# Kernel optimization log

Hardware: AMD Instinct MI355X
Metric: run time of the kernel (lower is better)

The kernel has to match this reference:

```python
import jax, jax.numpy as jnp
import numpy as np

# Hard-coded constants from the original module
GAMMA = 0.1      # self.gamma default
N_STEPS = 10     # self.n_steps default
RHO = 0.9        # RMSProp decay
LR = 0.009       # RMSProp learning rate
MOM = 0.9        # momentum
EPS = 1e-8       # RMSProp epsilon
ABS_EPS = 1e-6   # diff_abs smoothing: diff_abs(x) = sqrt(x^2 + 1e-6)

B, IN_DIM, OUT_DIM = 4096, 2048, 4096


def setup_inputs() -> dict:
    key = jax.random.key(0)
    k1, k2 = jax.random.split(key)
    inputs = jax.random.normal(k1, (B, IN_DIM), dtype=jnp.float32)
    # keras 'uniform' init: U(-0.05, 0.05), shape (output_dim, input_dim)
    W = jax.random.uniform(k2, (OUT_DIM, IN_DIM), minval=-0.05, maxval=0.05, dtype=jnp.float32)
    return {"inputs": inputs, "W": W}


def reference(inputs, W):
    batch = inputs.shape[0]
    out_dim = W.shape[0]
    a = jnp.sqrt(inputs * inputs + ABS_EPS)          # diff_abs(inputs), [B, in_dim]
    act = lambda u: 0.5 * (1.0 + jnp.exp(-u))        # self.activation

    def cost(x):
        # l1_norm.sum() + l1_inov + own_norm  (prior = 0)
        l1 = (GAMMA * act(x @ W) * a).sum()
        l1_inov = (GAMMA / 10.0) * jnp.sum(x * x)
        own = GAMMA * jnp.sum(jnp.sqrt(x * x + ABS_EPS))
        return l1 + l1_inov + own

    grad_cost = jax.grad(cost)

    def step(carry, _):
        x, acc1, acc2 = carry
        g = grad_cost(x)                              # [B, out_dim]
        new_acc1 = RHO * acc1 + (1.0 - RHO) * g * g
        denom = jnp.sqrt(new_acc1 + EPS)
        new_acc2 = MOM * acc2 - LR * g / denom
        cand = x - LR * g / denom
        t = 0.1 * LR / denom                          # elementwise prox threshold
        new_x = jnp.maximum(cand - t, 0.0) + jnp.minimum(cand + t, 0.0) + MOM * new_acc2
        new_x = jax.lax.stop_gradient(new_x)          # theano disconnected_grad
        return (new_x, new_acc1, new_acc2), None

    z = jnp.zeros((batch, out_dim), dtype=inputs.dtype)
    # scan runs n_steps; last step's l1_norm uses the state after n_steps-1 updates,
    # so run n_steps-1 updates then compute the final l1_norm directly.
    (x, _, _), _ = jax.lax.scan(step, (z, z, z), None, length=N_STEPS - 1)
    return GAMMA * act(x @ W) * a                     # outputs[-1][-1]: last l1_norm, [B, in_dim]
```

## Files before the change

kernel.cpp:

```cpp
#include <hip/hip_runtime.h>
#include <cstdint>
#include <cstddef>

#define B_DIM   4096
#define IN_DIM  2048
#define OUT_DIM 4096

typedef __attribute__((ext_vector_type(8))) __bf16 bf16x8;
typedef __attribute__((ext_vector_type(4))) float  f32x4;
typedef unsigned short ushortT;

__device__ __forceinline__ ushortT f2bf(float f) {
    unsigned int u = __float_as_uint(f);
    u += 0x7FFFu + ((u >> 16) & 1u);
    return (ushortT)(u >> 16);
}
__device__ __forceinline__ float bf2f(ushortT b) {
    return __uint_as_float(((unsigned int)b) << 16);
}

__device__ __forceinline__ void gload16(const void* g, void* l) {
    __builtin_amdgcn_global_load_lds(
        (const __attribute__((address_space(1))) void*)g,
        (__attribute__((address_space(3))) void*)l, 16, 0, 0);
}

__global__ void prep_g0_kernel(const float* __restrict__ in, ushortT* __restrict__ Gb,
                               ushortT* __restrict__ negA) {
    int i = blockIdx.x * 256 + threadIdx.x;
    float4 v = reinterpret_cast<const float4*>(in)[i];
    ushort4 g;
    g.x = f2bf(-0.05f * sqrtf(v.x * v.x + 1e-6f));
    g.y = f2bf(-0.05f * sqrtf(v.y * v.y + 1e-6f));
    g.z = f2bf(-0.05f * sqrtf(v.z * v.z + 1e-6f));
    g.w = f2bf(-0.05f * sqrtf(v.w * v.w + 1e-6f));
    reinterpret_cast<ushort4*>(Gb)[i]   = g;
    reinterpret_cast<ushort4*>(negA)[i] = g;
}

__global__ void conv_w_kernel(const float* __restrict__ W, ushortT* __restrict__ Wb,
                              ushortT* __restrict__ WTb) {
    __shared__ float tile[64][65];
    const int i0 = blockIdx.x * 64;
    const int j0 = blockIdx.y * 64;
    const int c  = threadIdx.x & 63;
    const int rq = threadIdx.x >> 6;
#pragma unroll
    for (int rp = 0; rp < 16; ++rp) {
        int row = rp * 4 + rq;
        float w = W[(size_t)(j0 + row) * IN_DIM + i0 + c];
        tile[row][c] = w;
        Wb[(size_t)(j0 + row) * IN_DIM + i0 + c] = f2bf(w);
    }
    __syncthreads();
#pragma unroll
    for (int rp = 0; rp < 16; ++rp) {
        int row = rp * 4 + rq;
        WTb[(size_t)(i0 + row) * OUT_DIM + j0 + c] = f2bf(tile[c][row]);
    }
}

#define EPILOGUE(MR_)                                                          \
    float* lep = (float*)(smem + w * 4352);                                    \
    const int li = lane >> 4;                                                  \
    const int lc = lane & 15;                                                  \
    _Pragma("unroll")                                                          \
    for (int m = 0; m < (MR_); ++m) {                                          \
        _Pragma("unroll")                                                      \
        for (int n = 0; n < 4; ++n)                                            \
            _Pragma("unroll")                                                  \
            for (int i = 0; i < 4; ++i)                                        \
                lep[(li * 4 + i) * 68 + n * 16 + lc] = acc[m][n][i];           \
        asm volatile("s_waitcnt lgkmcnt(0)" ::: "memory");                     \
        __builtin_amdgcn_sched_barrier(0);                                     \
        _Pragma("unroll")                                                      \
        for (int rr = 0; rr < 4; ++rr) {                                       \
            const int row = rr + li * 4;                                       \
            float4 v = *reinterpret_cast<const float4*>(&lep[row * 68 + lc * 4]); \
            const size_t idx  = (size_t)(row0w + m * 16 + row) * N + col0w + lc * 4; \
            const size_t idx4 = idx >> 2;                                      \
            if constexpr (EPI == 0) {                                          \
                ushort4 au = *reinterpret_cast<const ushort4*>(&nega[idx]);    \
                ushort4 g;                                                     \
                g.x = f2bf(bf2f(au.x) * __expf(-v.x));                         \
                g.y = f2bf(bf2f(au.y) * __expf(-v.y));                         \
                g.z = f2bf(bf2f(au.z) * __expf(-v.z));                         \
                g.w = f2bf(bf2f(au.w) * __expf(-v.w));                         \
                *reinterpret_cast<ushort4*>(&Gb[idx]) = g;                     \
            } else if constexpr (EPI == 1) {                                   \
                float4 iv = reinterpret_cast<const float4*>(inb)[idx4];        \
                float4 o;                                                      \
                o.x = 0.05f * (1.0f + expf(-v.x)) * sqrtf(iv.x * iv.x + 1e-6f); \
                o.y = 0.05f * (1.0f + expf(-v.y)) * sqrtf(iv.y * iv.y + 1e-6f); \
                o.z = 0.05f * (1.0f + expf(-v.z)) * sqrtf(iv.z * iv.z + 1e-6f); \
                o.w = 0.05f * (1.0f + expf(-v.w)) * sqrtf(iv.w * iv.w + 1e-6f); \
                reinterpret_cast<float4*>(out)[idx4] = o;                      \
            } else if constexpr (EPI == 3) {                                   \
                float vs[4] = {v.x, v.y, v.z, v.w};                            \
                ushortT a1n[4], a2n[4], xbn[4];                                \
                _Pragma("unroll")                                              \
                for (int j = 0; j < 4; ++j) {                                  \
                    float g    = vs[j];                                        \
                    float a1   = 0.1f * g * g;                                 \
                    float inv  = rsqrtf(a1 + 1e-8f);                           \
                    float r_   = 0.009f * g * inv;                             \
                    float a2   = -r_;                                          \
                    float cand = -r_;                                          \
                    float t_   = 0.0009f * inv;                                \
                    float xn   = fmaxf(cand - t_, 0.0f) + fminf(cand + t_, 0.0f) + 0.9f * a2; \
                    a1n[j] = f2bf(a1); a2n[j] = f2bf(a2); xbn[j] = f2bf(xn);   \
                }                                                              \
                *reinterpret_cast<ushort4*>(&acc1[idx]) = make_ushort4(a1n[0], a1n[1], a1n[2], a1n[3]); \
                *reinterpret_cast<ushort4*>(&acc2[idx]) = make_ushort4(a2n[0], a2n[1], a2n[2], a2n[3]); \
                *reinterpret_cast<ushort4*>(&xb[idx])   = make_ushort4(xbn[0], xbn[1], xbn[2], xbn[3]); \
            } else {                                                           \
                ushort4 xu  = *reinterpret_cast<const ushort4*>(&xb[idx]);     \
                ushort4 a1u = *reinterpret_cast<const ushort4*>(&acc1[idx]);   \
                ushort4 a2u = *reinterpret_cast<const ushort4*>(&acc2[idx]);   \
                float xs[4] = {bf2f(xu.x), bf2f(xu.y), bf2f(xu.z), bf2f(xu.w)}; \
                float vs[4] = {v.x, v.y, v.z, v.w};                            \
                ushortT a1s[4] = {a1u.x, a1u.y, a1u.z, a1u.w};                 \
                ushortT a2s[4] = {a2u.x, a2u.y, a2u.z, a2u.w};                 \
                ushortT a1n[4], a2n[4], xbn[4];                                \
                _Pragma("unroll")                                              \
                for (int j = 0; j < 4; ++j) {                                  \
                    float g    = vs[j] + 0.02f * xs[j] + 0.1f * xs[j] * rsqrtf(xs[j] * xs[j] + 1e-6f); \
                    float a1   = 0.9f * bf2f(a1s[j]) + 0.1f * g * g;           \
                    float inv  = rsqrtf(a1 + 1e-8f);                           \
                    float r_   = 0.009f * g * inv;                             \
                    float a2   = 0.9f * bf2f(a2s[j]) - r_;                     \
                    float cand = xs[j] - r_;                                   \
                    float t_   = 0.0009f * inv;                                \
                    float xn   = fmaxf(cand - t_, 0.0f) + fminf(cand + t_, 0.0f) + 0.9f * a2; \
                    a1n[j] = f2bf(a1); a2n[j] = f2bf(a2); xbn[j] = f2bf(xn);   \
                }                                                              \
                *reinterpret_cast<ushort4*>(&acc1[idx]) = make_ushort4(a1n[0], a1n[1], a1n[2], a1n[3]); \
                *reinterpret_cast<ushort4*>(&acc2[idx]) = make_ushort4(a2n[0], a2n[1], a2n[2], a2n[3]); \
                *reinterpret_cast<ushort4*>(&xb[idx])   = make_ushort4(xbn[0], xbn[1], xbn[2], xbn[3]); \
            }                                                                  \
        }                                                                      \
        asm volatile("s_waitcnt lgkmcnt(0)" ::: "memory");                     \
    }

#define PHASE(MB, RB, SLOTP, STTILE, C0, NC)                                   \
    {                                                                          \
        const char* sb_ = (SLOTP);                                             \
        if (RB) {                                                              \
            _Pragma("unroll")                                                  \
            for (int n = 0; n < 4; ++n)                                        \
                bF[n] = *reinterpret_cast<const bf16x8*>(sb_ + bRd[n]);        \
        }                                                                      \
        bf16x8 aF[4];                                                          \
        _Pragma("unroll")                                                      \
        for (int m = 0; m < 4; ++m)                                            \
            aF[m] = *reinterpret_cast<const bf16x8*>(sb_ + aRd[m]);            \
        if ((STTILE) < nt) {                                                   \
            _Pragma("unroll")                                                  \
            for (int c = 0; c < (NC); ++c) stage_chunk((STTILE), (C0) + c);    \
        }                                                                      \
        __builtin_amdgcn_sched_barrier(0);                                     \
        __builtin_amdgcn_s_barrier();                                          \
        asm volatile("s_waitcnt lgkmcnt(0)" ::: "memory");                     \
        __builtin_amdgcn_sched_barrier(0);                                     \
        __builtin_amdgcn_s_setprio(1);                                         \
        _Pragma("unroll")                                                      \
        for (int m = 0; m < 4; ++m) {                                          \
            _Pragma("unroll")                                                  \
            for (int n = 0; n < 4; ++n)                                        \
                acc[m][n] = __builtin_amdgcn_mfma_f32_16x16x32_bf16(           \
                    aF[m], bF[n], acc[m][n], 0, 0, 0);                         \
        }                                                                      \
        __builtin_amdgcn_s_setprio(0);                                         \
        __builtin_amdgcn_s_barrier();                                          \
        __builtin_amdgcn_sched_barrier(0);                                     \
    }

template <int EPI>
__global__ __launch_bounds__(512, 1)
void gemm_phase(const ushortT* __restrict__ A, const ushortT* __restrict__ Bm,
                int N, int K,
                const float* __restrict__ inb, const ushortT* __restrict__ nega,
                ushortT* __restrict__ Gb, float* __restrict__ out,
                ushortT* __restrict__ acc1, ushortT* __restrict__ acc2,
                ushortT* __restrict__ xb) {
    constexpr int BM = 128, BN = 256;
    constexpr int ASZ  = BM * 64;
    constexpr int SLOT = ASZ + BN * 64;
    constexpr int LA   = 1, LB = 2, L = 3;
    __shared__ alignas(16) char smem[4 * SLOT];

    const int tid  = threadIdx.x;
    const int lane = tid & 63;
    const int w    = tid >> 6;
    const int wm   = w >> 2;
    const int wn   = w & 3;
    const int nbx  = N / BN;
    const int nwg  = gridDim.x;
    const int cpx  = nwg >> 3;
    const int bid  = (int)blockIdx.x;
    const int swz  = (bid & 7) * cpx + (bid >> 3);
    const int bx   = swz % nbx;
    const int by   = swz / nbx;
    const int row0 = by * BM;
    const int col0 = bx * BN;
    const size_t strideK2 = (size_t)K * 2;

    const char* gp[L]; int lo[L];
#pragma unroll
    for (int i = 0; i < LA; ++i) {
        int Lp  = i * 512 + tid;
        int row = Lp >> 2, sl = Lp & 3;
        int src = sl ^ ((row >> 1) & 3);
        gp[i] = (const char*)A + (size_t)(row0 + row) * strideK2 + src * 16;
        lo[i] = i * 8192 + w * 1024;
    }
#pragma unroll
    for (int i = 0; i < LB; ++i) {
        int Lp  = i * 512 + tid;
        int row = Lp >> 2, sl = Lp & 3;
        int src = sl ^ ((row >> 1) & 3);
        gp[LA + i] = (const char*)Bm + (size_t)(col0 + row) * strideK2 + src * 16;
        lo[LA + i] = ASZ + i * 8192 + w * 1024;
    }
    auto stage_all = [&](int tt) {
        char* sb = smem + (tt & 3) * SLOT;
        const size_t kb = (size_t)tt * 64;
#pragma unroll
        for (int c = 0; c < L; ++c) gload16(gp[c] + kb, sb + lo[c]);
    };
    auto stage_chunk = [&](int tt, int c) {
        gload16(gp[c] + (size_t)tt * 64, smem + (tt & 3) * SLOT + lo[c]);
    };

    int aRd[4], bRd[4];
#pragma unroll
    for (int m = 0; m < 4; ++m) {
        int row = wm * 64 + m * 16 + (lane & 15);
        aRd[m] = row * 64 + (((lane >> 4) ^ ((row >> 1) & 3)) * 16);
    }
#pragma unroll
    for (int n = 0; n < 4; ++n) {
        int row = wn * 64 + n * 16 + (lane & 15);
        bRd[n] = ASZ + row * 64 + (((lane >> 4) ^ ((row >> 1) & 3)) * 16);
    }

    f32x4 acc[4][4] = {};
    const int nt = K >> 5;

    stage_all(0); stage_all(1); stage_all(2);

    for (int tt = 0; tt < nt; tt += 2) {
        if (tt + 2 < nt) asm volatile("s_waitcnt vmcnt(%0)" :: "n"(L) : "memory");
        else             asm volatile("s_waitcnt vmcnt(0)"  ::: "memory");
        __builtin_amdgcn_s_barrier();
        __builtin_amdgcn_sched_barrier(0);

        const char* sb0 = smem + (tt & 3) * SLOT;
        const char* sb1 = smem + ((tt + 1) & 3) * SLOT;
        bf16x8 bF[4];
        PHASE(0, true, sb0, tt + 3, 0, 3)
        PHASE(0, true, sb1, tt + 4, 0, 3)
    }

    __builtin_amdgcn_s_barrier();
    const int row0w = row0 + wm * 64;
    const int col0w = col0 + wn * 64;
    EPILOGUE(4)
}

template <int EPI>
__global__ __launch_bounds__(512, 4)
void gemm_mb(const ushortT* __restrict__ A, const ushortT* __restrict__ Bm,
             int N, int K,
             const float* __restrict__ inb, const ushortT* __restrict__ nega,
             ushortT* __restrict__ Gb, float* __restrict__ out,
             ushortT* __restrict__ acc1, ushortT* __restrict__ acc2,
             ushortT* __restrict__ xb) {
    constexpr int BM = 256, BN = 128;
    constexpr int ASZ  = BM * 64;
    constexpr int SLOT = ASZ + BN * 64;
    constexpr int CA   = 2, CB = 1, L = 3;
    __shared__ alignas(16) char smem[3 * SLOT];

    const int tid  = threadIdx.x;
    const int lane = tid & 63;
    const int w    = tid >> 6;
    const int wm   = w >> 1;
    const int wn   = w & 1;
    const int nbx  = N / BN;
    const int nwg  = gridDim.x;
    const int cpx  = nwg >> 3;
    const int bid  = (int)blockIdx.x;
    const int swz  = (bid & 7) * cpx + (bid >> 3);
    const int bx   = swz % nbx;
    const int by   = swz / nbx;
    const int row0 = by * BM;
    const int col0 = bx * BN;
    const size_t strideK2 = (size_t)K * 2;

    const char* gp[L]; int lo[L];
#pragma unroll
    for (int c = 0; c < CA; ++c) {
        int Lp  = c * 512 + tid;
        int row = Lp >> 2, sl = Lp & 3;
        int src = sl ^ ((row >> 1) & 3);
        gp[c] = (const char*)A + (size_t)(row0 + row) * strideK2 + src * 16;
        lo[c] = c * 8192 + w * 1024;
    }
#pragma unroll
    for (int c = 0; c < CB; ++c) {
        int Lp  = c * 512 + tid;
        int row = Lp >> 2, sl = Lp & 3;
        int src = sl ^ ((row >> 1) & 3);
        gp[CA + c] = (const char*)Bm + (size_t)(col0 + row) * strideK2 + src * 16;
        lo[CA + c] = ASZ + c * 8192 + w * 1024;
    }
    auto stage = [&](int tt) {
        char* sb = smem + (tt % 3) * SLOT;
        const size_t kb = (size_t)tt * 64;
#pragma unroll
        for (int c = 0; c < L; ++c) gload16(gp[c] + kb, sb + lo[c]);
    };

    int aRd[4], bRd[4];
#pragma unroll
    for (int m = 0; m < 4; ++m) {
        int row = wm * 64 + m * 16 + (lane & 15);
        aRd[m] = row * 64 + (((lane >> 4) ^ ((row >> 1) & 3)) * 16);
    }
#pragma unroll
    for (int n = 0; n < 4; ++n) {
        int row = wn * 64 + n * 16 + (lane & 15);
        bRd[n] = ASZ + row * 64 + (((lane >> 4) ^ ((row >> 1) & 3)) * 16);
    }

    f32x4 acc[4][4] = {};
    const int nt = K >> 5;

    stage(0); stage(1);

    for (int tt = 0; tt < nt; ++tt) {
        if (tt < nt - 1) asm volatile("s_waitcnt vmcnt(%0)" :: "n"(L) : "memory");
        else             asm volatile("s_waitcnt vmcnt(0)"  ::: "memory");
        __builtin_amdgcn_s_barrier();
        __builtin_amdgcn_sched_barrier(0);

        const char* sb = smem + (tt % 3) * SLOT;
        bf16x8 aF[4], bF[4];
#pragma unroll
        for (int n = 0; n < 4; ++n) bF[n] = *reinterpret_cast<const bf16x8*>(sb + bRd[n]);
#pragma unroll
        for (int m = 0; m < 4; ++m) aF[m] = *reinterpret_cast<const bf16x8*>(sb + aRd[m]);
        if (tt + 2 < nt) stage(tt + 2);
        __builtin_amdgcn_s_setprio(1);
#pragma unroll
        for (int m = 0; m < 4; ++m)
#pragma unroll
            for (int n = 0; n < 4; ++n)
                acc[m][n] = __builtin_amdgcn_mfma_f32_16x16x32_bf16(aF[m], bF[n], acc[m][n], 0, 0, 0);
        __builtin_amdgcn_s_setprio(0);
    }

    __builtin_amdgcn_s_barrier();
    const int row0w = row0 + wm * 64;
    const int col0w = col0 + wn * 64;
    EPILOGUE(4)
}

extern "C" void kernel_launch(void* const* d_in, const int* in_sizes, int n_in,
                              void* d_out, int out_size, void* d_ws, size_t ws_size,
                              hipStream_t stream) {
    const float* in = (const float*)d_in[0];
    const float* W  = (const float*)d_in[1];
    float* out = (float*)d_out;
    char* ws = (char*)d_ws;

    ushortT* acc1 = (ushortT*)(ws);
    ushortT* acc2 = (ushortT*)(ws + ((size_t)32  << 20));
    ushortT* xb   = (ushortT*)(ws + ((size_t)64  << 20));
    ushortT* Wb   = (ushortT*)(ws + ((size_t)96  << 20));
    ushortT* WTb  = (ushortT*)(ws + ((size_t)112 << 20));
    ushortT* Gb   = (ushortT*)(ws + ((size_t)128 << 20));
    ushortT* negA = (ushortT*)(ws + ((size_t)144 << 20));


    prep_g0_kernel<<<dim3(B_DIM * IN_DIM / 4 / 256), dim3(256), 0, stream>>>(in, Gb, negA);
    conv_w_kernel<<<dim3(IN_DIM / 64, OUT_DIM / 64), dim3(256), 0, stream>>>(W, Wb, WTb);

    gemm_mb<3><<<dim3(512), dim3(512), 0, stream>>>(
        Gb, Wb, OUT_DIM, IN_DIM, nullptr, nullptr, nullptr, nullptr, acc1, acc2, xb);
    for (int step = 1; step < 9; ++step) {
        gemm_phase<0><<<dim3(256), dim3(512), 0, stream>>>(
            xb, WTb, IN_DIM, OUT_DIM, nullptr, negA, Gb, nullptr, nullptr, nullptr, nullptr);
        gemm_mb<2><<<dim3(512), dim3(512), 0, stream>>>(
            Gb, Wb, OUT_DIM, IN_DIM, nullptr, nullptr, nullptr, nullptr, acc1, acc2, xb);
    }
    gemm_phase<1><<<dim3(256), dim3(512), 0, stream>>>(
        xb, WTb, IN_DIM, OUT_DIM, in, nullptr, nullptr, out, nullptr, nullptr, nullptr);
}
```

Measured before the change: 1.533 ms.

## Load A operand fragments directly from global memory, staging only B in LDS

Both GEMM kernels now read the A-operand MFMA fragments straight from global memory into registers each k-tile, and use LDS only for the B operand. This shrinks LDS footprint and shared-memory traffic and removes the A staging loads. The cost is that A loads become uncoalesced per-lane 16-byte global reads that sit on the critical path before the MFMAs with no prefetch depth. gemm_da also adds a barrier at the end of every iteration.

```diff
diff --git a/kernel.cpp b/kernel.cpp
--- a/kernel.cpp
+++ b/kernel.cpp
@@ -142,21 +142,19 @@
         asm volatile("s_waitcnt lgkmcnt(0)" ::: "memory");                     \
     }
 
-#define PHASE(MB, RB, SLOTP, STTILE, C0, NC)                                   \
+#define PHASE_DA(TK, SLOTP, STTILE)                                            \
     {                                                                          \
         const char* sb_ = (SLOTP);                                             \
-        if (RB) {                                                              \
-            _Pragma("unroll")                                                  \
-            for (int n = 0; n < 4; ++n)                                        \
-                bF[n] = *reinterpret_cast<const bf16x8*>(sb_ + bRd[n]);        \
-        }                                                                      \
-        bf16x8 aF[4];                                                          \
+        bf16x8 aF[4], bF[4];                                                   \
         _Pragma("unroll")                                                      \
         for (int m = 0; m < 4; ++m)                                            \
-            aF[m] = *reinterpret_cast<const bf16x8*>(sb_ + aRd[m]);            \
+            aF[m] = *reinterpret_cast<const bf16x8*>(gAf[m] + (size_t)(TK) * 64); \
+        _Pragma("unroll")                                                      \
+        for (int n = 0; n < 4; ++n)                                            \
+            bF[n] = *reinterpret_cast<const bf16x8*>(sb_ + bRd[n]);            \
         if ((STTILE) < nt) {                                                   \
-            _Pragma("unroll")                                                  \
-            for (int c = 0; c < (NC); ++c) stage_chunk((STTILE), (C0) + c);    \
+            gload16(gp[0] + (size_t)(STTILE) * 64, smem + ((STTILE) & 3) * SLOT + lo[0]); \
+            gload16(gp[1] + (size_t)(STTILE) * 64, smem + ((STTILE) & 3) * SLOT + lo[1]); \
         }                                                                      \
         __builtin_amdgcn_sched_barrier(0);                                     \
         __builtin_amdgcn_s_barrier();                                          \
@@ -184,9 +182,7 @@
                 ushortT* __restrict__ acc1, ushortT* __restrict__ acc2,
                 ushortT* __restrict__ xb) {
     constexpr int BM = 128, BN = 256;
-    constexpr int ASZ  = BM * 64;
-    constexpr int SLOT = ASZ + BN * 64;
-    constexpr int LA   = 1, LB = 2, L = 3;
+    constexpr int SLOT = BN * 64;
     __shared__ alignas(16) char smem[4 * SLOT];
 
     const int tid  = threadIdx.x;
@@ -205,43 +201,33 @@
     const int col0 = bx * BN;
     const size_t strideK2 = (size_t)K * 2;
 
-    const char* gp[L]; int lo[L];
-#pragma unroll
-    for (int i = 0; i < LA; ++i) {
+    const char* gp[2]; int lo[2];
+#pragma unroll
+    for (int i = 0; i < 2; ++i) {
         int Lp  = i * 512 + tid;
         int row = Lp >> 2, sl = Lp & 3;
         int src = sl ^ ((row >> 1) & 3);
-        gp[i] = (const char*)A + (size_t)(row0 + row) * strideK2 + src * 16;
+        gp[i] = (const char*)Bm + (size_t)(col0 + row) * strideK2 + src * 16;
         lo[i] = i * 8192 + w * 1024;
-    }
-#pragma unroll
-    for (int i = 0; i < LB; ++i) {
-        int Lp  = i * 512 + tid;
-        int row = Lp >> 2, sl = Lp & 3;
-        int src = sl ^ ((row >> 1) & 3);
-        gp[LA + i] = (const char*)Bm + (size_t)(col0 + row) * strideK2 + src * 16;
-        lo[LA + i] = ASZ + i * 8192 + w * 1024;
     }
     auto stage_all = [&](int tt) {
         char* sb = smem + (tt & 3) * SLOT;
         const size_t kb = (size_t)tt * 64;
-#pragma unroll
-        for (int c = 0; c < L; ++c) gload16(gp[c] + kb, sb + lo[c]);
+        gload16(gp[0] + kb, sb + lo[0]);
+        gload16(gp[1] + kb, sb + lo[1]);
     };
-    auto stage_chunk = [&](int tt, int c) {
-        gload16(gp[c] + (size_t)tt * 64, smem + (tt & 3) * SLOT + lo[c]);
-    };
-
-    int aRd[4], bRd[4];
-#pragma unroll
-    for (int m = 0; m < 4; ++m) {
-        int row = wm * 64 + m * 16 + (lane & 15);
-        aRd[m] = row * 64 + (((lane >> 4) ^ ((row >> 1) & 3)) * 16);
-    }
+
+    int bRd[4];
 #pragma unroll
     for (int n = 0; n < 4; ++n) {
         int row = wn * 64 + n * 16 + (lane & 15);
-        bRd[n] = ASZ + row * 64 + (((lane >> 4) ^ ((row >> 1) & 3)) * 16);
+        bRd[n] = row * 64 + (((lane >> 4) ^ ((row >> 1) & 3)) * 16);
+    }
+    const char* gAf[4];
+#pragma unroll
+    for (int m = 0; m < 4; ++m) {
+        int rowA = row0 + wm * 64 + m * 16 + (lane & 15);
+        gAf[m] = (const char*)A + (size_t)rowA * strideK2 + (lane >> 4) * 16;
     }
 
     f32x4 acc[4][4] = {};
@@ -250,16 +236,15 @@
     stage_all(0); stage_all(1); stage_all(2);
 
     for (int tt = 0; tt < nt; tt += 2) {
-        if (tt + 2 < nt) asm volatile("s_waitcnt vmcnt(%0)" :: "n"(L) : "memory");
-        else             asm volatile("s_waitcnt vmcnt(0)"  ::: "memory");
+        if (tt + 2 < nt) asm volatile("s_waitcnt vmcnt(2)" ::: "memory");
+        else             asm volatile("s_waitcnt vmcnt(0)" ::: "memory");
         __builtin_amdgcn_s_barrier();
         __builtin_amdgcn_sched_barrier(0);
 
         const char* sb0 = smem + (tt & 3) * SLOT;
         const char* sb1 = smem + ((tt + 1) & 3) * SLOT;
-        bf16x8 bF[4];
-        PHASE(0, true, sb0, tt + 3, 0, 3)
-        PHASE(0, true, sb1, tt + 4, 0, 3)
+        PHASE_DA(tt,     sb0, tt + 3)
+        PHASE_DA(tt + 1, sb1, tt + 4)
     }
 
     __builtin_amdgcn_s_barrier();
@@ -270,17 +255,15 @@
 
 template <int EPI>
 __global__ __launch_bounds__(512, 4)
-void gemm_mb(const ushortT* __restrict__ A, const ushortT* __restrict__ Bm,
+void gemm_da(const ushortT* __restrict__ A, const ushortT* __restrict__ Bm,
              int N, int K,
              const float* __restrict__ inb, const ushortT* __restrict__ nega,
              ushortT* __restrict__ Gb, float* __restrict__ out,
              ushortT* __restrict__ acc1, ushortT* __restrict__ acc2,
              ushortT* __restrict__ xb) {
     constexpr int BM = 256, BN = 128;
-    constexpr int ASZ  = BM * 64;
-    constexpr int SLOT = ASZ + BN * 64;
-    constexpr int CA   = 2, CB = 1, L = 3;
-    __shared__ alignas(16) char smem[3 * SLOT];
+    constexpr int BSZ = BN * 64;
+    __shared__ alignas(16) char smem[34816];
 
     const int tid  = threadIdx.x;
     const int lane = tid & 63;
@@ -298,60 +281,49 @@
     const int col0 = bx * BN;
     const size_t strideK2 = (size_t)K * 2;
 
-    const char* gp[L]; int lo[L];
-#pragma unroll
-    for (int c = 0; c < CA; ++c) {
-        int Lp  = c * 512 + tid;
-        int row = Lp >> 2, sl = Lp & 3;
-        int src = sl ^ ((row >> 1) & 3);
-        gp[c] = (const char*)A + (size_t)(row0 + row) * strideK2 + src * 16;
-        lo[c] = c * 8192 + w * 1024;
-    }
-#pragma unroll
-    for (int c = 0; c < CB; ++c) {
-        int Lp  = c * 512 + tid;
-        int row = Lp >> 2, sl = Lp & 3;
-        int src = sl ^ ((row >> 1) & 3);
-        gp[CA + c] = (const char*)Bm + (size_t)(col0 + row) * strideK2 + src * 16;
-        lo[CA + c] = ASZ + c * 8192 + w * 1024;
-    }
-    auto stage = [&](int tt) {
-        char* sb = smem + (tt % 3) * SLOT;
-        const size_t kb = (size_t)tt * 64;
-#pragma unroll
-        for (int c = 0; c < L; ++c) gload16(gp[c] + kb, sb + lo[c]);
+    {
+    }
+    const int rowS = tid >> 2;
+    const int srcS = (tid & 3) ^ ((rowS >> 1) & 3);
+    const char* gB = (const char*)Bm + (size_t)(col0 + rowS) * strideK2 + srcS * 16;
+    const int loB = w * 1024;
+    auto stageB = [&](int tt) {
+        gload16(gB + (size_t)tt * 64, smem + (tt % 3) * BSZ + loB);
     };
 
-    int aRd[4], bRd[4];
-#pragma unroll
-    for (int m = 0; m < 4; ++m) {
-        int row = wm * 64 + m * 16 + (lane & 15);
-        aRd[m] = row * 64 + (((lane >> 4) ^ ((row >> 1) & 3)) * 16);
-    }
+    int bRd[4];
 #pragma unroll
     for (int n = 0; n < 4; ++n) {
         int row = wn * 64 + n * 16 + (lane & 15);
-        bRd[n] = ASZ + row * 64 + (((lane >> 4) ^ ((row >> 1) & 3)) * 16);
+        bRd[n] = row * 64 + (((lane >> 4) ^ ((row >> 1) & 3)) * 16);
+    }
+    const char* gAf[4];
+#pragma unroll
+    for (int m = 0; m < 4; ++m) {
+        int rowA = row0 + wm * 64 + m * 16 + (lane & 15);
+        gAf[m] = (const char*)A + (size_t)rowA * strideK2 + (lane >> 4) * 16;
     }
 
     f32x4 acc[4][4] = {};
     const int nt = K >> 5;
 
-    stage(0); stage(1);
+    stageB(0); stageB(1);
 
     for (int tt = 0; tt < nt; ++tt) {
-        if (tt < nt - 1) asm volatile("s_waitcnt vmcnt(%0)" :: "n"(L) : "memory");
-        else             asm volatile("s_waitcnt vmcnt(0)"  ::: "memory");
+        if (tt < nt - 1) asm volatile("s_waitcnt vmcnt(1)" ::: "memory");
+        else             asm volatile("s_waitcnt vmcnt(0)" ::: "memory");
         __builtin_amdgcn_s_barrier();
         __builtin_amdgcn_sched_barrier(0);
 
-        const char* sb = smem + (tt % 3) * SLOT;
+        const char* sb = smem + (tt % 3) * BSZ;
         bf16x8 aF[4], bF[4];
 #pragma unroll
-        for (int n = 0; n < 4; ++n) bF[n] = *reinterpret_cast<const bf16x8*>(sb + bRd[n]);
-#pragma unroll
-        for (int m = 0; m < 4; ++m) aF[m] = *reinterpret_cast<const bf16x8*>(sb + aRd[m]);
-        if (tt + 2 < nt) stage(tt + 2);
+        for (int m = 0; m < 4; ++m)
+            aF[m] = *reinterpret_cast<const bf16x8*>(gAf[m] + (size_t)tt * 64);
+#pragma unroll
+        for (int n = 0; n < 4; ++n)
+            bF[n] = *reinterpret_cast<const bf16x8*>(sb + bRd[n]);
+        if (tt + 2 < nt) stageB(tt + 2);
         __builtin_amdgcn_s_setprio(1);
 #pragma unroll
         for (int m = 0; m < 4; ++m)
@@ -359,9 +331,10 @@
             for (int n = 0; n < 4; ++n)
                 acc[m][n] = __builtin_amdgcn_mfma_f32_16x16x32_bf16(aF[m], bF[n], acc[m][n], 0, 0, 0);
         __builtin_amdgcn_s_setprio(0);
-    }
-
-    __builtin_amdgcn_s_barrier();
+        __builtin_amdgcn_s_barrier();
+        __builtin_amdgcn_sched_barrier(0);
+    }
+
     const int row0w = row0 + wm * 64;
     const int col0w = col0 + wn * 64;
     EPILOGUE(4)
@@ -387,12 +360,12 @@
     prep_g0_kernel<<<dim3(B_DIM * IN_DIM / 4 / 256), dim3(256), 0, stream>>>(in, Gb, negA);
     conv_w_kernel<<<dim3(IN_DIM / 64, OUT_DIM / 64), dim3(256), 0, stream>>>(W, Wb, WTb);
 
-    gemm_mb<3><<<dim3(512), dim3(512), 0, stream>>>(
+    gemm_da<3><<<dim3(512), dim3(512), 0, stream>>>(
         Gb, Wb, OUT_DIM, IN_DIM, nullptr, nullptr, nullptr, nullptr, acc1, acc2, xb);
     for (int step = 1; step < 9; ++step) {
         gemm_phase<0><<<dim3(256), dim3(512), 0, stream>>>(
             xb, WTb, IN_DIM, OUT_DIM, nullptr, negA, Gb, nullptr, nullptr, nullptr, nullptr);
-        gemm_mb<2><<<dim3(512), dim3(512), 0, stream>>>(
+        gemm_da<2><<<dim3(512), dim3(512), 0, stream>>>(
             Gb, Wb, OUT_DIM, IN_DIM, nullptr, nullptr, nullptr, nullptr, acc1, acc2, xb);
     }
     gemm_phase<1><<<dim3(256), dim3(512), 0, stream>>>(
```

Measured after the change: 2.941 ms. +91.8%, slower.
